# Optimization experiments

Hardware: AMD Instinct MI355X
Metric: run time of the kernel (lower is better)

The kernel has to match this reference:

```python
import jax, jax.numpy as jnp
import numpy as np

D = 1024
H = 16
HD = D // H
EPS = 1e-5


def layer_norm(x, g, b):
    mu = jnp.mean(x, axis=-1, keepdims=True)
    var = jnp.mean((x - mu) ** 2, axis=-1, keepdims=True)
    return (x - mu) * jax.lax.rsqrt(var + EPS) * g + b


def setup_inputs() -> dict:
    key = jax.random.key(0)
    ks = jax.random.split(key, 10)
    s = lambda fan_in: 1.0 / np.sqrt(fan_in)
    inp = {
        "x": jax.random.normal(ks[0], (2, 2048, D), dtype=jnp.float32),
        "w_qkv": jax.random.uniform(ks[1], (D, 3 * D), minval=-s(D), maxval=s(D)),
        "b_qkv": jnp.zeros((3 * D,), jnp.float32),
        "w_fc": jax.random.uniform(ks[2], (D, D), minval=-s(D), maxval=s(D)),
        "b_fc": jnp.zeros((D,), jnp.float32),
        "ln1_g": jnp.ones((D,), jnp.float32),
        "ln1_b": jnp.zeros((D,), jnp.float32),
        "ln2_g": jnp.ones((D,), jnp.float32),
        "ln2_b": jnp.zeros((D,), jnp.float32),
        "w1": jax.random.uniform(ks[3], (D, 4 * D), minval=-s(D), maxval=s(D)),
        "b1": jnp.zeros((4 * D,), jnp.float32),
        "w2": jax.random.uniform(ks[4], (4 * D, D), minval=-s(4 * D), maxval=s(4 * D)),
        "b2": jnp.zeros((D,), jnp.float32),
    }
    return inp


def reference(x, w_qkv, b_qkv, w_fc, b_fc, ln1_g, ln1_b, ln2_g, ln2_b, w1, b1, w2, b2):
    B, T, C = x.shape
    # --- attention sublayer (pre-norm) ---
    h = layer_norm(x, ln1_g, ln1_b)
    qkv = (h @ w_qkv + b_qkv).reshape(B, T, 3, H, HD)
    q, k, v = qkv[:, :, 0], qkv[:, :, 1], qkv[:, :, 2]  # [B,T,H,HD]
    scores = jnp.einsum("bqhd,bkhd->bhqk", q, k) / np.sqrt(HD).astype(np.float32)
    causal = jnp.tril(jnp.ones((T, T), dtype=bool))
    scores = jnp.where(causal, scores, -jnp.inf)
    weights = jax.nn.softmax(scores, axis=-1)
    out = jnp.einsum("bhqk,bkhd->bqhd", weights, v).reshape(B, T, C)
    x = x + out @ w_fc + b_fc
    # --- MLP sublayer (pre-norm) ---
    h = layer_norm(x, ln2_g, ln2_b)
    h = jax.nn.gelu(h @ w1 + b1, approximate=False) @ w2 + b2
    return x + h
```

## Files before the change

kernel.cpp:

```cpp
#include <hip/hip_runtime.h>
#include <hip/hip_bf16.h>
#include <cstdint>
#include <cstddef>

#define SEQ 2048
#define DM  1024

typedef __attribute__((ext_vector_type(8))) __bf16 bf16x8;
typedef __attribute__((ext_vector_type(4))) float  f32x4;
using bf16 = __hip_bfloat16;

__device__ __forceinline__ void gload_lds16(const bf16* g, bf16* l) {
  __builtin_amdgcn_global_load_lds((const __attribute__((address_space(1))) void*)g,
                                   (__attribute__((address_space(3))) void*)l,
                                   16, 0, 0);
}

__global__ void transpose_to_bf16(const float* __restrict__ in, bf16* __restrict__ out,
                                  int K, int N) {
  __shared__ float tile[32][33];
  const int k0 = blockIdx.y * 32, n0 = blockIdx.x * 32;
  const int tx = threadIdx.x, ty = threadIdx.y;
#pragma unroll
  for (int i = ty; i < 32; i += 8)
    tile[i][tx] = in[(size_t)(k0 + i) * N + n0 + tx];
  __syncthreads();
#pragma unroll
  for (int i = ty; i < 32; i += 8)
    out[(size_t)(n0 + i) * K + k0 + tx] = __float2bfloat16(tile[tx][i]);
}

__global__ void ln_to_bf16(const float* __restrict__ x, const float* __restrict__ g,
                           const float* __restrict__ bt, bf16* __restrict__ out) {
  const int row = blockIdx.x;
  const float4 v = ((const float4*)(x + (size_t)row * DM))[threadIdx.x];
  float s  = v.x + v.y + v.z + v.w;
  float s2 = v.x * v.x + v.y * v.y + v.z * v.z + v.w * v.w;
#pragma unroll
  for (int o = 32; o > 0; o >>= 1) { s += __shfl_down(s, o); s2 += __shfl_down(s2, o); }
  __shared__ float red[8];
  const int wave = threadIdx.x >> 6, lane = threadIdx.x & 63;
  if (lane == 0) { red[wave] = s; red[4 + wave] = s2; }
  __syncthreads();
  s  = red[0] + red[1] + red[2] + red[3];
  s2 = red[4] + red[5] + red[6] + red[7];
  const float mu  = s * (1.f / DM);
  const float var = s2 * (1.f / DM) - mu * mu;
  const float r   = rsqrtf(var + 1e-5f);
  const float4 gv = ((const float4*)g)[threadIdx.x];
  const float4 bv = ((const float4*)bt)[threadIdx.x];
  bf16* o = out + (size_t)row * DM + threadIdx.x * 4;
  o[0] = __float2bfloat16((v.x - mu) * r * gv.x + bv.x);
  o[1] = __float2bfloat16((v.y - mu) * r * gv.y + bv.y);
  o[2] = __float2bfloat16((v.z - mu) * r * gv.z + bv.z);
  o[3] = __float2bfloat16((v.w - mu) * r * gv.w + bv.w);
}

enum { EP_BF16 = 0, EP_GELU = 1, EP_RESID = 2, EP_QKV = 3 };

template <int MODE, int TM, int TN>
__global__ void gemm_bt(const bf16* __restrict__ A, const bf16* __restrict__ Bt,
                        const float* __restrict__ bias, const float* __restrict__ resid,
                        float* __restrict__ Cf, bf16* __restrict__ Cb, bf16* __restrict__ vt,
                        int M, int N, int K) {
  constexpr int ABUF = TM * 32;
  constexpr int BBUF = TN * 32;
  constexpr int MI = TM / 32;
  constexpr int NI = TN / 32;
  __shared__ __attribute__((aligned(16))) bf16 As[2 * ABUF];
  __shared__ __attribute__((aligned(16))) bf16 Bs[2 * BBUF];
  const int tid  = threadIdx.x;
  const int wave = tid >> 6, lane = tid & 63;
  const int l16 = lane & 15, lq = lane >> 4;
  const int m0 = blockIdx.x * TM, n0 = blockIdx.y * TN;
  const int wr = (wave >> 1) * (TM / 2), wc = (wave & 1) * (TN / 2);

  f32x4 acc[MI][NI];
#pragma unroll
  for (int i = 0; i < MI; i++)
#pragma unroll
    for (int j = 0; j < NI; j++) acc[i][j] = 0;

  const int srow = tid >> 2;
  const int scol = (tid & 3) * 8;
  const bf16* ga = A  + (size_t)(m0 + srow) * K + scol;
  const bf16* gb = Bt + (size_t)(n0 + srow) * K + scol;

  {
    bf16* la = As + wave * 512;
    bf16* lb = Bs + wave * 512;
    gload_lds16(ga, la);
    if (TM == 128) gload_lds16(ga + (size_t)64 * K, la + 2048);
    gload_lds16(gb, lb);
    if (TN == 128) gload_lds16(gb + (size_t)64 * K, lb + 2048);
  }

  const int NKT = K >> 5;
  for (int it = 0; it < NKT; ++it) {
    __syncthreads();
    const int cur = it & 1, nxt = cur ^ 1;
    if (it + 1 < NKT) {
      const int kt = (it + 1) << 5;
      bf16* la = As + nxt * ABUF + wave * 512;
      bf16* lb = Bs + nxt * BBUF + wave * 512;
      gload_lds16(ga + kt, la);
      if (TM == 128) gload_lds16(ga + (size_t)64 * K + kt, la + 2048);
      gload_lds16(gb + kt, lb);
      if (TN == 128) gload_lds16(gb + (size_t)64 * K + kt, lb + 2048);
    }
    bf16x8 af[MI], bfr[NI];
#pragma unroll
    for (int mi = 0; mi < MI; mi++)
      af[mi] = *(const bf16x8*)(As + cur * ABUF + (wr + mi * 16 + l16) * 32 + lq * 8);
#pragma unroll
    for (int ni = 0; ni < NI; ni++)
      bfr[ni] = *(const bf16x8*)(Bs + cur * BBUF + (wc + ni * 16 + l16) * 32 + lq * 8);
#pragma unroll
    for (int mi = 0; mi < MI; mi++)
#pragma unroll
      for (int ni = 0; ni < NI; ni++)
        acc[mi][ni] = __builtin_amdgcn_mfma_f32_16x16x32_bf16(af[mi], bfr[ni], acc[mi][ni], 0, 0, 0);
  }

#pragma unroll
  for (int ni = 0; ni < NI; ni++) {
    const int col = n0 + wc + ni * 16 + l16;
    const float bb = bias[col];
#pragma unroll
    for (int mi = 0; mi < MI; mi++) {
      if constexpr (MODE == EP_QKV) {
        const int row0 = m0 + wr + mi * 16 + lq * 4;
        if (col >= 2048) {
          __attribute__((aligned(8))) bf16 pk[4];
#pragma unroll
          for (int r = 0; r < 4; r++) pk[r] = __float2bfloat16(acc[mi][ni][r] + bb);
          *(uint2*)(vt + (size_t)((row0 >> 11) * 1024 + (col - 2048)) * SEQ + (row0 & 2047)) =
              *(const uint2*)pk;
        } else {
#pragma unroll
          for (int r = 0; r < 4; r++)
            Cb[(size_t)(row0 + r) * N + col] = __float2bfloat16(acc[mi][ni][r] + bb);
        }
      } else {
#pragma unroll
        for (int r = 0; r < 4; r++) {
          const int row = m0 + wr + mi * 16 + lq * 4 + r;
          const size_t idx = (size_t)row * N + col;
          float v = acc[mi][ni][r] + bb;
          if (MODE == EP_BF16) {
            Cb[idx] = __float2bfloat16(v);
          } else if (MODE == EP_GELU) {
            v = 0.5f * v * (1.0f + erff(v * 0.70710678118654752f));
            Cb[idx] = __float2bfloat16(v);
          } else {
            Cf[idx] = resid[idx] + v;
          }
        }
      }
    }
  }
}

__global__ __launch_bounds__(256, 4)
void gemm_bt64(const bf16* __restrict__ A, const bf16* __restrict__ Bt,
               const float* __restrict__ bias, const float* __restrict__ resid,
               float* __restrict__ Cf, int M, int N, int K) {
  constexpr int TILE = 64 * 64;
  __shared__ __attribute__((aligned(16))) bf16 As[2 * TILE];
  __shared__ __attribute__((aligned(16))) bf16 Bs[2 * TILE];
  const int tid  = threadIdx.x;
  const int wave = tid >> 6, lane = tid & 63;
  const int l16 = lane & 15, lq = lane >> 4;
  const int m0 = blockIdx.x * 64, n0 = blockIdx.y * 64;
  const int wr = (wave >> 1) * 32, wc = (wave & 1) * 32;

  f32x4 acc[2][2];
#pragma unroll
  for (int i = 0; i < 2; i++)
#pragma unroll
    for (int j = 0; j < 2; j++) acc[i][j] = 0;

  const int srow = tid >> 3;
  const int scb  = (tid & 7) ^ (srow & 7);
  const bf16* ga0 = A  + (size_t)(m0 + srow) * K + scb * 8;
  const bf16* ga1 = A  + (size_t)(m0 + srow + 32) * K + scb * 8;
  const bf16* gb0 = Bt + (size_t)(n0 + srow) * K + scb * 8;
  const bf16* gb1 = Bt + (size_t)(n0 + srow + 32) * K + scb * 8;
  const int ld0 = wave * 512;
  const int ld1 = 2048 + wave * 512;

  gload_lds16(ga0, As + ld0);
  gload_lds16(ga1, As + ld1);
  gload_lds16(gb0, Bs + ld0);
  gload_lds16(gb1, Bs + ld1);

  const int sxa = l16 & 7;

  const int NKT = K >> 6;
  for (int it = 0; it < NKT; ++it) {
    __syncthreads();
    const int cur = (it & 1) * TILE;
    if (it + 1 < NKT) {
      const int nxt = ((it + 1) & 1) * TILE;
      const int kt = (it + 1) << 6;
      gload_lds16(ga0 + kt, As + nxt + ld0);
      gload_lds16(ga1 + kt, As + nxt + ld1);
      gload_lds16(gb0 + kt, Bs + nxt + ld0);
      gload_lds16(gb1 + kt, Bs + nxt + ld1);
    }
    bf16x8 af[2][2], bfv[2][2];
#pragma unroll
    for (int mi = 0; mi < 2; mi++) {
      const int row = wr + mi * 16 + l16;
#pragma unroll
      for (int kk = 0; kk < 2; kk++)
        af[mi][kk] = *(const bf16x8*)(As + cur + row * 64 + (((kk * 4 + lq) ^ sxa) << 3));
    }
#pragma unroll
    for (int ni = 0; ni < 2; ni++) {
      const int row = wc + ni * 16 + l16;
#pragma unroll
      for (int kk = 0; kk < 2; kk++)
        bfv[ni][kk] = *(const bf16x8*)(Bs + cur + row * 64 + (((kk * 4 + lq) ^ sxa) << 3));
    }
#pragma unroll
    for (int kk = 0; kk < 2; kk++)
#pragma unroll
      for (int mi = 0; mi < 2; mi++)
#pragma unroll
        for (int ni = 0; ni < 2; ni++)
          acc[mi][ni] = __builtin_amdgcn_mfma_f32_16x16x32_bf16(af[mi][kk], bfv[ni][kk],
                                                                acc[mi][ni], 0, 0, 0);
  }

#pragma unroll
  for (int ni = 0; ni < 2; ni++) {
    const int col = n0 + wc + ni * 16 + l16;
    const float bb = bias[col];
#pragma unroll
    for (int mi = 0; mi < 2; mi++) {
#pragma unroll
      for (int r = 0; r < 4; r++) {
        const int row = m0 + wr + mi * 16 + lq * 4 + r;
        const size_t idx = (size_t)row * N + col;
        Cf[idx] = resid[idx] + acc[mi][ni][r] + bb;
      }
    }
  }
}

#define SCALE_LOG2 0.18033688011112042f

__global__ __launch_bounds__(512, 2)
void flash_attn(const bf16* __restrict__ qkv, const bf16* __restrict__ VTg,
                bf16* __restrict__ out) {
  const int idx  = blockIdx.x;
  const int praw = idx & 15;
  const int p    = ((idx >> 8) & 1) ? (15 - praw) : praw;
  const int bh   = (idx >> 4) & 31;
  const int h    = bh & 15;
  const int b    = bh >> 4;
  const int qlow = p, qhigh = 31 - p;

  const int tid = threadIdx.x;
  const int w = tid >> 6, lane = tid & 63;
  const int wq = w & 3, hf = w >> 2;
  const int l16 = lane & 15, lq = lane >> 4;
  const int myqb = hf ? qlow : qhigh;

  const size_t base = (size_t)b * SEQ * 3072;
  const bf16* Qg = qkv + base + (size_t)h * 64;
  const bf16* Kg = qkv + base + 1024 + (size_t)h * 64;
  const bf16* Vt = VTg + (size_t)(b * 1024 + h * 64) * SEQ;

  __shared__ __attribute__((aligned(16))) bf16 Ks[2 * 4096];
  __shared__ __attribute__((aligned(16))) bf16 VTs[2 * 4096];
  __shared__ __attribute__((aligned(16))) bf16 Ps[8 * 1024];

  const int srow = tid >> 3;
  const int scb  = (tid & 7) ^ (srow & 7);
  const bf16* gK = Kg + (size_t)srow * 3072 + scb * 8;
  const bf16* gV = Vt + (size_t)srow * SEQ + scb * 8;
  const int ldst = w * 512;

  gload_lds16(gK, Ks + ldst);
  gload_lds16(gV, VTs + ldst);

  const bf16* qrow = Qg + (size_t)(myqb * 64 + wq * 16 + l16) * 3072 + lq * 8;
  const bf16x8 qf0 = *(const bf16x8*)(qrow);
  const bf16x8 qf1 = *(const bf16x8*)(qrow + 32);

  const int koffA = l16 * 64 + ((lq ^ (l16 & 7)) << 3);
  const int koffB = l16 * 64 + (((4 + lq) ^ (l16 & 7)) << 3);
  const int l16h = l16 >> 3;
  const int pco  = w * 1024 + (l16 & 7);

  f32x4 oacc[4];
#pragma unroll
  for (int i = 0; i < 4; i++) oacc[i] = 0;
  float lsum[4] = {0.f, 0.f, 0.f, 0.f};

  const int nkt = qhigh + 1;
  for (int kb = 0; kb < nkt; ++kb) {
    __syncthreads();
    const int cur = (kb & 1) * 4096;
    if (kb + 1 < nkt) {
      const int nxt = ((kb + 1) & 1) * 4096;
      const size_t ko = (size_t)(kb + 1) * 64;
      gload_lds16(gK + ko * 3072, Ks + nxt + ldst);
      gload_lds16(gV + ko, VTs + nxt + ldst);
    }

    if (kb <= myqb) {
      f32x4 sacc[4];
#pragma unroll
      for (int nt = 0; nt < 4; nt++) sacc[nt] = 0;
#pragma unroll
      for (int nt = 0; nt < 4; nt++) {
        const bf16x8 kf0 = *(const bf16x8*)(Ks + cur + nt * 1024 + koffA);
        const bf16x8 kf1 = *(const bf16x8*)(Ks + cur + nt * 1024 + koffB);
        sacc[nt] = __builtin_amdgcn_mfma_f32_16x16x32_bf16(qf0, kf0, sacc[nt], 0, 0, 0);
        sacc[nt] = __builtin_amdgcn_mfma_f32_16x16x32_bf16(qf1, kf1, sacc[nt], 0, 0, 0);
      }

      if (kb == myqb) {
#pragma unroll
        for (int r = 0; r < 4; r++) {
          const int rowp = lq * 4 + r;
          const int qloc = wq * 16 + rowp;
          float e[4];
#pragma unroll
          for (int nt = 0; nt < 4; nt++) {
            float sv = sacc[nt][r] * SCALE_LOG2;
            sv = fminf(sv, 88.f);
            if (nt * 16 + l16 > qloc) sv = -1e30f;
            e[nt] = exp2f(sv);
            Ps[pco + rowp * 64 + ((((nt * 2 + l16h)) ^ (rowp & 7)) << 3)] = __float2bfloat16(e[nt]);
          }
          lsum[r] += (e[0] + e[1]) + (e[2] + e[3]);
        }
      } else {
#pragma unroll
        for (int r = 0; r < 4; r++) {
          const int rowp = lq * 4 + r;
          float e[4];
#pragma unroll
          for (int nt = 0; nt < 4; nt++) {
            float sv = sacc[nt][r] * SCALE_LOG2;
            sv = fminf(sv, 88.f);
            e[nt] = exp2f(sv);
            Ps[pco + rowp * 64 + ((((nt * 2 + l16h)) ^ (rowp & 7)) << 3)] = __float2bfloat16(e[nt]);
          }
          lsum[r] += (e[0] + e[1]) + (e[2] + e[3]);
        }
      }

      const bf16x8 pf0 = *(const bf16x8*)(Ps + w * 1024 + koffA);
      const bf16x8 pf1 = *(const bf16x8*)(Ps + w * 1024 + koffB);
#pragma unroll
      for (int dt = 0; dt < 4; dt++) {
        const bf16x8 vf0 = *(const bf16x8*)(VTs + cur + dt * 1024 + koffA);
        const bf16x8 vf1 = *(const bf16x8*)(VTs + cur + dt * 1024 + koffB);
        oacc[dt] = __builtin_amdgcn_mfma_f32_16x16x32_bf16(pf0, vf0, oacc[dt], 0, 0, 0);
        oacc[dt] = __builtin_amdgcn_mfma_f32_16x16x32_bf16(pf1, vf1, oacc[dt], 0, 0, 0);
      }
    }
  }

#pragma unroll
  for (int r = 0; r < 4; r++) {
    float l = lsum[r];
    l += __shfl_xor(l, 1);
    l += __shfl_xor(l, 2);
    l += __shfl_xor(l, 4);
    l += __shfl_xor(l, 8);
    lsum[r] = 1.f / l;
  }
#pragma unroll
  for (int dt = 0; dt < 4; dt++)
#pragma unroll
    for (int r = 0; r < 4; r++) {
      const int qrow_ = myqb * 64 + wq * 16 + lq * 4 + r;
      const float v = oacc[dt][r] * lsum[r];
      out[(size_t)(b * SEQ + qrow_) * DM + h * 64 + dt * 16 + l16] = __float2bfloat16(v);
    }
}

extern "C" void kernel_launch(void* const* d_in, const int* in_sizes, int n_in,
                              void* d_out, int out_size, void* d_ws, size_t ws_size,
                              hipStream_t stream) {
  const float* x     = (const float*)d_in[0];
  const float* w_qkv = (const float*)d_in[1];
  const float* b_qkv = (const float*)d_in[2];
  const float* w_fc  = (const float*)d_in[3];
  const float* b_fc  = (const float*)d_in[4];
  const float* ln1_g = (const float*)d_in[5];
  const float* ln1_b = (const float*)d_in[6];
  const float* ln2_g = (const float*)d_in[7];
  const float* ln2_b = (const float*)d_in[8];
  const float* w1    = (const float*)d_in[9];
  const float* b1    = (const float*)d_in[10];
  const float* w2    = (const float*)d_in[11];
  const float* b2    = (const float*)d_in[12];
  float* out = (float*)d_out;

  char* ws    = (char*)d_ws;
  float* x2   = (float*)(ws);
  bf16* VTg   = (bf16*)(ws);
  bf16* big   = (bf16*)(ws + (size_t)(16 << 20));
  bf16* small = (bf16*)(ws + (size_t)(48 << 20));
  bf16* wT    = (bf16*)(ws + (size_t)(56 << 20));

  const dim3 tb(32, 8);

  ln_to_bf16<<<dim3(4096), dim3(256), 0, stream>>>(x, ln1_g, ln1_b, small);
  transpose_to_bf16<<<dim3(96, 32), tb, 0, stream>>>(w_qkv, wT, 1024, 3072);
  gemm_bt<EP_QKV, 128, 128><<<dim3(32, 24), dim3(256), 0, stream>>>(
      small, wT, b_qkv, nullptr, nullptr, big, VTg, 4096, 3072, 1024);
  flash_attn<<<dim3(512), dim3(512), 0, stream>>>(big, VTg, small);
  transpose_to_bf16<<<dim3(32, 32), tb, 0, stream>>>(w_fc, wT, 1024, 1024);
  gemm_bt64<<<dim3(64, 16), dim3(256), 0, stream>>>(
      small, wT, b_fc, x, x2, 4096, 1024, 1024);
  ln_to_bf16<<<dim3(4096), dim3(256), 0, stream>>>(x2, ln2_g, ln2_b, small);
  transpose_to_bf16<<<dim3(128, 32), tb, 0, stream>>>(w1, wT, 1024, 4096);
  gemm_bt<EP_GELU, 128, 128><<<dim3(32, 32), dim3(256), 0, stream>>>(
      small, wT, b1, nullptr, nullptr, big, nullptr, 4096, 4096, 1024);
  transpose_to_bf16<<<dim3(32, 128), tb, 0, stream>>>(w2, wT, 4096, 1024);
  gemm_bt64<<<dim3(64, 16), dim3(256), 0, stream>>>(
      big, wT, b2, x2, out, 4096, 1024, 4096);
}
```

Baseline: 351.7 us.

## Triple-buffer GEMM LDS staging with explicit vmcnt waits and two-ahead prefetch

Both bf16 GEMM kernels move from double to triple LDS buffering. Global-to-LDS loads are now issued two k-tiles ahead. The implicit full wait before each barrier is replaced with s_waitcnt vmcnt(4), so the loads for the next tile can stay in flight while the current tile is computed. The intent is to hide more global-memory latency behind MFMA work. In exchange, LDS use goes up by half, the occupancy hint drops to 3 blocks, and the hard-coded vmcnt(4) is only correct when each stage issues exactly four loads; tile shapes with 64-wide tiles issue fewer and could read incomplete data.

```diff
diff --git a/kernel.cpp b/kernel.cpp
--- a/kernel.cpp
+++ b/kernel.cpp
@@ -14,6 +14,12 @@
   __builtin_amdgcn_global_load_lds((const __attribute__((address_space(1))) void*)g,
                                    (__attribute__((address_space(3))) void*)l,
                                    16, 0, 0);
+}
+__device__ __forceinline__ void vm_wait4() { asm volatile("s_waitcnt vmcnt(4)" ::: "memory"); }
+__device__ __forceinline__ void vm_wait0() { asm volatile("s_waitcnt vmcnt(0)" ::: "memory"); }
+__device__ __forceinline__ void pipe_barrier() {
+  __builtin_amdgcn_s_barrier();
+  __builtin_amdgcn_sched_barrier(0);
 }
 
 __global__ void transpose_to_bf16(const float* __restrict__ in, bf16* __restrict__ out,
@@ -59,16 +65,17 @@
 enum { EP_BF16 = 0, EP_GELU = 1, EP_RESID = 2, EP_QKV = 3 };
 
 template <int MODE, int TM, int TN>
-__global__ void gemm_bt(const bf16* __restrict__ A, const bf16* __restrict__ Bt,
-                        const float* __restrict__ bias, const float* __restrict__ resid,
-                        float* __restrict__ Cf, bf16* __restrict__ Cb, bf16* __restrict__ vt,
-                        int M, int N, int K) {
+__global__ __launch_bounds__(256, 3)
+void gemm_bt(const bf16* __restrict__ A, const bf16* __restrict__ Bt,
+             const float* __restrict__ bias, const float* __restrict__ resid,
+             float* __restrict__ Cf, bf16* __restrict__ Cb, bf16* __restrict__ vt,
+             int M, int N, int K) {
   constexpr int ABUF = TM * 32;
   constexpr int BBUF = TN * 32;
   constexpr int MI = TM / 32;
   constexpr int NI = TN / 32;
-  __shared__ __attribute__((aligned(16))) bf16 As[2 * ABUF];
-  __shared__ __attribute__((aligned(16))) bf16 Bs[2 * BBUF];
+  __shared__ __attribute__((aligned(16))) bf16 As[3 * ABUF];
+  __shared__ __attribute__((aligned(16))) bf16 Bs[3 * BBUF];
   const int tid  = threadIdx.x;
   const int wave = tid >> 6, lane = tid & 63;
   const int l16 = lane & 15, lq = lane >> 4;
@@ -86,40 +93,41 @@
   const bf16* ga = A  + (size_t)(m0 + srow) * K + scol;
   const bf16* gb = Bt + (size_t)(n0 + srow) * K + scol;
 
-  {
-    bf16* la = As + wave * 512;
-    bf16* lb = Bs + wave * 512;
-    gload_lds16(ga, la);
-    if (TM == 128) gload_lds16(ga + (size_t)64 * K, la + 2048);
-    gload_lds16(gb, lb);
-    if (TN == 128) gload_lds16(gb + (size_t)64 * K, lb + 2048);
-  }
+  auto stage = [&](int t, int buf) {
+    const int kt = t << 5;
+    bf16* la = As + buf * ABUF + wave * 512;
+    bf16* lb = Bs + buf * BBUF + wave * 512;
+    gload_lds16(ga + kt, la);
+    if (TM == 128) gload_lds16(ga + (size_t)64 * K + kt, la + 2048);
+    gload_lds16(gb + kt, lb);
+    if (TN == 128) gload_lds16(gb + (size_t)64 * K + kt, lb + 2048);
+  };
 
   const int NKT = K >> 5;
+  stage(0, 0);
+  if (NKT > 1) stage(1, 1);
+
+  int bc = 0, bs = 2;
   for (int it = 0; it < NKT; ++it) {
-    __syncthreads();
-    const int cur = it & 1, nxt = cur ^ 1;
-    if (it + 1 < NKT) {
-      const int kt = (it + 1) << 5;
-      bf16* la = As + nxt * ABUF + wave * 512;
-      bf16* lb = Bs + nxt * BBUF + wave * 512;
-      gload_lds16(ga + kt, la);
-      if (TM == 128) gload_lds16(ga + (size_t)64 * K + kt, la + 2048);
-      gload_lds16(gb + kt, lb);
-      if (TN == 128) gload_lds16(gb + (size_t)64 * K + kt, lb + 2048);
-    }
+    if (it + 1 < NKT) vm_wait4(); else vm_wait0();
+    pipe_barrier();
+    if (it + 2 < NKT) stage(it + 2, bs);
+
     bf16x8 af[MI], bfr[NI];
 #pragma unroll
     for (int mi = 0; mi < MI; mi++)
-      af[mi] = *(const bf16x8*)(As + cur * ABUF + (wr + mi * 16 + l16) * 32 + lq * 8);
+      af[mi] = *(const bf16x8*)(As + bc * ABUF + (wr + mi * 16 + l16) * 32 + lq * 8);
 #pragma unroll
     for (int ni = 0; ni < NI; ni++)
-      bfr[ni] = *(const bf16x8*)(Bs + cur * BBUF + (wc + ni * 16 + l16) * 32 + lq * 8);
+      bfr[ni] = *(const bf16x8*)(Bs + bc * BBUF + (wc + ni * 16 + l16) * 32 + lq * 8);
 #pragma unroll
     for (int mi = 0; mi < MI; mi++)
 #pragma unroll
       for (int ni = 0; ni < NI; ni++)
         acc[mi][ni] = __builtin_amdgcn_mfma_f32_16x16x32_bf16(af[mi], bfr[ni], acc[mi][ni], 0, 0, 0);
+
+    bc = (bc == 2) ? 0 : bc + 1;
+    bs = (bs == 2) ? 0 : bs + 1;
   }
 
 #pragma unroll
@@ -161,13 +169,13 @@
   }
 }
 
-__global__ __launch_bounds__(256, 4)
+__global__ __launch_bounds__(256, 3)
 void gemm_bt64(const bf16* __restrict__ A, const bf16* __restrict__ Bt,
                const float* __restrict__ bias, const float* __restrict__ resid,
                float* __restrict__ Cf, int M, int N, int K) {
   constexpr int TILE = 64 * 64;
-  __shared__ __attribute__((aligned(16))) bf16 As[2 * TILE];
-  __shared__ __attribute__((aligned(16))) bf16 Bs[2 * TILE];
+  __shared__ __attribute__((aligned(16))) bf16 As[3 * TILE];
+  __shared__ __attribute__((aligned(16))) bf16 Bs[3 * TILE];
   const int tid  = threadIdx.x;
   const int wave = tid >> 6, lane = tid & 63;
   const int l16 = lane & 15, lq = lane >> 4;
@@ -189,25 +197,27 @@
   const int ld0 = wave * 512;
   const int ld1 = 2048 + wave * 512;
 
-  gload_lds16(ga0, As + ld0);
-  gload_lds16(ga1, As + ld1);
-  gload_lds16(gb0, Bs + ld0);
-  gload_lds16(gb1, Bs + ld1);
+  auto stage = [&](int t, int buf) {
+    const int kt = t << 6;
+    gload_lds16(ga0 + kt, As + buf * TILE + ld0);
+    gload_lds16(ga1 + kt, As + buf * TILE + ld1);
+    gload_lds16(gb0 + kt, Bs + buf * TILE + ld0);
+    gload_lds16(gb1 + kt, Bs + buf * TILE + ld1);
+  };
 
   const int sxa = l16 & 7;
 
   const int NKT = K >> 6;
+  stage(0, 0);
+  if (NKT > 1) stage(1, 1);
+
+  int bc = 0, bs = 2;
   for (int it = 0; it < NKT; ++it) {
-    __syncthreads();
-    const int cur = (it & 1) * TILE;
-    if (it + 1 < NKT) {
-      const int nxt = ((it + 1) & 1) * TILE;
-      const int kt = (it + 1) << 6;
-      gload_lds16(ga0 + kt, As + nxt + ld0);
-      gload_lds16(ga1 + kt, As + nxt + ld1);
-      gload_lds16(gb0 + kt, Bs + nxt + ld0);
-      gload_lds16(gb1 + kt, Bs + nxt + ld1);
-    }
+    if (it + 1 < NKT) vm_wait4(); else vm_wait0();
+    pipe_barrier();
+    if (it + 2 < NKT) stage(it + 2, bs);
+
+    const int cur = bc * TILE;
     bf16x8 af[2][2], bfv[2][2];
 #pragma unroll
     for (int mi = 0; mi < 2; mi++) {
@@ -231,6 +241,9 @@
         for (int ni = 0; ni < 2; ni++)
           acc[mi][ni] = __builtin_amdgcn_mfma_f32_16x16x32_bf16(af[mi][kk], bfv[ni][kk],
                                                                 acc[mi][ni], 0, 0, 0);
+
+    bc = (bc == 2) ? 0 : bc + 1;
+    bs = (bs == 2) ? 0 : bs + 1;
   }
 
 #pragma unroll
```

After: 400.0 us. +13.7%, slower.

## Replace 128x128 GEMM with 256x128 tile, BK=64, swizzled LDS, triple-buffered A

Applied to the files above, without the earlier changes.

The QKV and MLP-up GEMMs move to a new 512-thread kernel with 256x128 output tiles and a K step of 64. LDS columns are XOR-swizzled to avoid bank conflicts. A is triple-buffered and B double-buffered, with explicit vmcnt waits plus barriers so loads stay in flight across iterations. MFMA blocks run at raised wave priority. The aim is more data reuse per tile and better overlap of memory and compute, at the cost of higher register and LDS use (about 128KB of LDS) and fewer blocks in the grid.

```diff
diff --git a/kernel.cpp b/kernel.cpp
--- a/kernel.cpp
+++ b/kernel.cpp
@@ -15,6 +15,8 @@
                                    (__attribute__((address_space(3))) void*)l,
                                    16, 0, 0);
 }
+__device__ __forceinline__ void wb4() { asm volatile("s_waitcnt vmcnt(4)\n\ts_barrier" ::: "memory"); }
+__device__ __forceinline__ void wb0() { asm volatile("s_waitcnt vmcnt(0)\n\ts_barrier" ::: "memory"); }
 
 __global__ void transpose_to_bf16(const float* __restrict__ in, bf16* __restrict__ out,
                                   int K, int N) {
@@ -58,76 +60,88 @@
 
 enum { EP_BF16 = 0, EP_GELU = 1, EP_RESID = 2, EP_QKV = 3 };
 
-template <int MODE, int TM, int TN>
-__global__ void gemm_bt(const bf16* __restrict__ A, const bf16* __restrict__ Bt,
-                        const float* __restrict__ bias, const float* __restrict__ resid,
-                        float* __restrict__ Cf, bf16* __restrict__ Cb, bf16* __restrict__ vt,
-                        int M, int N, int K) {
-  constexpr int ABUF = TM * 32;
-  constexpr int BBUF = TN * 32;
-  constexpr int MI = TM / 32;
-  constexpr int NI = TN / 32;
-  __shared__ __attribute__((aligned(16))) bf16 As[2 * ABUF];
-  __shared__ __attribute__((aligned(16))) bf16 Bs[2 * BBUF];
-  const int tid  = threadIdx.x;
-  const int wave = tid >> 6, lane = tid & 63;
+template <int MODE>
+__global__ __launch_bounds__(512, 2)
+void gemm256(const bf16* __restrict__ A, const bf16* __restrict__ Bt,
+             const float* __restrict__ bias,
+             bf16* __restrict__ Cb, bf16* __restrict__ vt,
+             int M, int N, int K) {
+  constexpr int ATILE = 256 * 64;
+  constexpr int BTILE = 128 * 64;
+  __shared__ __attribute__((aligned(16))) bf16 As[3 * ATILE];
+  __shared__ __attribute__((aligned(16))) bf16 Bs[2 * BTILE];
+  const int tid = threadIdx.x;
+  const int w = tid >> 6, lane = tid & 63;
   const int l16 = lane & 15, lq = lane >> 4;
-  const int m0 = blockIdx.x * TM, n0 = blockIdx.y * TN;
-  const int wr = (wave >> 1) * (TM / 2), wc = (wave & 1) * (TN / 2);
-
-  f32x4 acc[MI][NI];
-#pragma unroll
-  for (int i = 0; i < MI; i++)
-#pragma unroll
-    for (int j = 0; j < NI; j++) acc[i][j] = 0;
-
-  const int srow = tid >> 2;
-  const int scol = (tid & 3) * 8;
-  const bf16* ga = A  + (size_t)(m0 + srow) * K + scol;
-  const bf16* gb = Bt + (size_t)(n0 + srow) * K + scol;
-
-  {
-    bf16* la = As + wave * 512;
-    bf16* lb = Bs + wave * 512;
-    gload_lds16(ga, la);
-    if (TM == 128) gload_lds16(ga + (size_t)64 * K, la + 2048);
-    gload_lds16(gb, lb);
-    if (TN == 128) gload_lds16(gb + (size_t)64 * K, lb + 2048);
-  }
-
-  const int NKT = K >> 5;
+  const int m0 = blockIdx.x * 256, n0 = blockIdx.y * 128;
+  const int wr = (w >> 1) * 64, wc = (w & 1) * 64;
+
+  f32x4 acc[4][4];
+#pragma unroll
+  for (int i = 0; i < 4; i++)
+#pragma unroll
+    for (int j = 0; j < 4; j++) acc[i][j] = 0;
+
+  const int srow = tid >> 3;
+  const int scb  = (tid & 7) ^ (srow & 7);
+  const bf16* gA = A  + (size_t)(m0 + srow) * K + scb * 8;
+  const bf16* gB = Bt + (size_t)(n0 + srow) * K + scb * 8;
+  const int lw = w * 512;
+
+  auto stageA = [&](int t) {
+    const int kt = t << 6;
+    bf16* d = As + (t % 3) * ATILE + lw;
+#pragma unroll
+    for (int i = 0; i < 4; i++)
+      gload_lds16(gA + (size_t)i * 64 * K + kt, d + i * 4096);
+  };
+  auto stageB = [&](int t) {
+    const int kt = t << 6;
+    bf16* d = Bs + (t & 1) * BTILE + lw;
+#pragma unroll
+    for (int j = 0; j < 2; j++)
+      gload_lds16(gB + (size_t)j * 64 * K + kt, d + j * 4096);
+  };
+
+  const int NKT = K >> 6;
+  stageB(0); stageA(0); stageA(1);
+
+  const int sxa = l16 & 7;
   for (int it = 0; it < NKT; ++it) {
-    __syncthreads();
-    const int cur = it & 1, nxt = cur ^ 1;
-    if (it + 1 < NKT) {
-      const int kt = (it + 1) << 5;
-      bf16* la = As + nxt * ABUF + wave * 512;
-      bf16* lb = Bs + nxt * BBUF + wave * 512;
-      gload_lds16(ga + kt, la);
-      if (TM == 128) gload_lds16(ga + (size_t)64 * K + kt, la + 2048);
-      gload_lds16(gb + kt, lb);
-      if (TN == 128) gload_lds16(gb + (size_t)64 * K + kt, lb + 2048);
-    }
-    bf16x8 af[MI], bfr[NI];
-#pragma unroll
-    for (int mi = 0; mi < MI; mi++)
-      af[mi] = *(const bf16x8*)(As + cur * ABUF + (wr + mi * 16 + l16) * 32 + lq * 8);
-#pragma unroll
-    for (int ni = 0; ni < NI; ni++)
-      bfr[ni] = *(const bf16x8*)(Bs + cur * BBUF + (wc + ni * 16 + l16) * 32 + lq * 8);
-#pragma unroll
-    for (int mi = 0; mi < MI; mi++)
-#pragma unroll
-      for (int ni = 0; ni < NI; ni++)
-        acc[mi][ni] = __builtin_amdgcn_mfma_f32_16x16x32_bf16(af[mi], bfr[ni], acc[mi][ni], 0, 0, 0);
-  }
-
-#pragma unroll
-  for (int ni = 0; ni < NI; ni++) {
+    if (it + 1 < NKT) wb4(); else wb0();
+    if (it + 1 < NKT) stageB(it + 1);
+    if (it + 2 < NKT) stageA(it + 2);
+    const bf16* a  = As + (it % 3) * ATILE;
+    const bf16* bb = Bs + (it & 1) * BTILE;
+#pragma unroll
+    for (int ks = 0; ks < 2; ks++) {
+      bf16x8 af[4], bfv[4];
+#pragma unroll
+      for (int mi = 0; mi < 4; mi++) {
+        const int row = wr + mi * 16 + l16;
+        af[mi] = *(const bf16x8*)(a + row * 64 + (((ks * 4 + lq) ^ sxa) << 3));
+      }
+#pragma unroll
+      for (int ni = 0; ni < 4; ni++) {
+        const int row = wc + ni * 16 + l16;
+        bfv[ni] = *(const bf16x8*)(bb + row * 64 + (((ks * 4 + lq) ^ sxa) << 3));
+      }
+      __builtin_amdgcn_s_setprio(1);
+#pragma unroll
+      for (int mi = 0; mi < 4; mi++)
+#pragma unroll
+        for (int ni = 0; ni < 4; ni++)
+          acc[mi][ni] = __builtin_amdgcn_mfma_f32_16x16x32_bf16(af[mi], bfv[ni], acc[mi][ni], 0, 0, 0);
+      __builtin_amdgcn_s_setprio(0);
+    }
+  }
+
+#pragma unroll
+  for (int ni = 0; ni < 4; ni++) {
     const int col = n0 + wc + ni * 16 + l16;
     const float bb = bias[col];
 #pragma unroll
-    for (int mi = 0; mi < MI; mi++) {
+    for (int mi = 0; mi < 4; mi++) {
       if constexpr (MODE == EP_QKV) {
         const int row0 = m0 + wr + mi * 16 + lq * 4;
         if (col >= 2048) {
@@ -145,16 +159,9 @@
 #pragma unroll
         for (int r = 0; r < 4; r++) {
           const int row = m0 + wr + mi * 16 + lq * 4 + r;
-          const size_t idx = (size_t)row * N + col;
           float v = acc[mi][ni][r] + bb;
-          if (MODE == EP_BF16) {
-            Cb[idx] = __float2bfloat16(v);
-          } else if (MODE == EP_GELU) {
-            v = 0.5f * v * (1.0f + erff(v * 0.70710678118654752f));
-            Cb[idx] = __float2bfloat16(v);
-          } else {
-            Cf[idx] = resid[idx] + v;
-          }
+          v = 0.5f * v * (1.0f + erff(v * 0.70710678118654752f));
+          Cb[(size_t)row * N + col] = __float2bfloat16(v);
         }
       }
     }
@@ -415,16 +422,16 @@
 
   ln_to_bf16<<<dim3(4096), dim3(256), 0, stream>>>(x, ln1_g, ln1_b, small);
   transpose_to_bf16<<<dim3(96, 32), tb, 0, stream>>>(w_qkv, wT, 1024, 3072);
-  gemm_bt<EP_QKV, 128, 128><<<dim3(32, 24), dim3(256), 0, stream>>>(
-      small, wT, b_qkv, nullptr, nullptr, big, VTg, 4096, 3072, 1024);
+  gemm256<EP_QKV><<<dim3(16, 24), dim3(512), 0, stream>>>(
+      small, wT, b_qkv, big, VTg, 4096, 3072, 1024);
   flash_attn<<<dim3(512), dim3(512), 0, stream>>>(big, VTg, small);
   transpose_to_bf16<<<dim3(32, 32), tb, 0, stream>>>(w_fc, wT, 1024, 1024);
   gemm_bt64<<<dim3(64, 16), dim3(256), 0, stream>>>(
       small, wT, b_fc, x, x2, 4096, 1024, 1024);
   ln_to_bf16<<<dim3(4096), dim3(256), 0, stream>>>(x2, ln2_g, ln2_b, small);
   transpose_to_bf16<<<dim3(128, 32), tb, 0, stream>>>(w1, wT, 1024, 4096);
-  gemm_bt<EP_GELU, 128, 128><<<dim3(32, 32), dim3(256), 0, stream>>>(
-      small, wT, b1, nullptr, nullptr, big, nullptr, 4096, 4096, 1024);
+  gemm256<EP_GELU><<<dim3(16, 32), dim3(512), 0, stream>>>(
+      small, wT, b1, big, nullptr, 4096, 4096, 1024);
   transpose_to_bf16<<<dim3(32, 128), tb, 0, stream>>>(w2, wT, 4096, 1024);
   gemm_bt64<<<dim3(64, 16), dim3(256), 0, stream>>>(
       big, wT, b2, x2, out, 4096, 1024, 4096);
```

Measured after the change: 376.2 us. +7.0%, slower.
